# Performance work log

Measured on AMD Instinct MI355X. Metric: run time of the kernel, lower is better.

The kernel has to match this reference:

```python
import jax, jax.numpy as jnp
import numpy as np

B, D, H, W = 2, 64, 128, 128
LARGE = 1e8  # sentinel squared distance (no surface found yet)


def setup_inputs() -> dict:
    key = jax.random.key(0)
    k1, k2 = jax.random.split(key)
    pred = jax.random.normal(k1, (B, 1, D, H, W), dtype=jnp.float32)
    # binary ground-truth mask stored as float, as in the torch module
    target = jax.random.randint(k2, (B, 1, D, H, W), 0, 2).astype(jnp.float32)
    return {"pred": pred, "target": target}


def _erode(m):
    """scipy.ndimage.binary_erosion with default 6-connectivity structure,
    border_value=0 (out-of-bounds treated as background)."""
    e = m
    for ax in range(3):
        pad = [(1, 1) if i == ax else (0, 0) for i in range(3)]
        p = jnp.pad(m, pad)  # False padding
        n = m.shape[ax]
        lo = jax.lax.slice_in_dim(p, 0, n, axis=ax)      # m[i-1]
        hi = jax.lax.slice_in_dim(p, 2, n + 2, axis=ax)  # m[i+1]
        e = e & lo & hi
    return e


def _edt_pass(d2, axis):
    """One separable pass of the exact squared EDT:
    out[i] = min_j (d2[j] + (i-j)^2) along `axis` (Felzenszwalb decomposition,
    computed by brute-force broadcast min, vectorized over all lines)."""
    moved = jnp.moveaxis(d2, axis, 0)
    moved_shape = moved.shape
    n = moved_shape[0]
    x = moved.reshape(n, -1)  # (n, rest)
    idx = jnp.arange(n, dtype=d2.dtype)
    diff2 = (idx[:, None] - idx[None, :]) ** 2  # (n_out, n_in)
    out = jnp.min(x[None, :, :] + diff2[:, :, None], axis=1)  # (n_out, rest)
    return jnp.moveaxis(out.reshape(moved_shape), 0, axis)


def _surface_distance(mask):
    """Distance from every voxel to the nearest surface voxel, where
    surface = mask & ~binary_erosion(mask). Matches
    ndimage.distance_transform_edt(~surface) (exact Euclidean)."""
    eroded = _erode(mask)
    surface = mask & ~eroded
    d2 = jnp.where(surface, jnp.float32(0.0), jnp.float32(LARGE))
    for ax in range(3):
        d2 = _edt_pass(d2, ax)
    return jnp.sqrt(d2)


def _smooth_l1(a, b):
    d = a - b
    ad = jnp.abs(d)
    return jnp.mean(jnp.where(ad < 1.0, 0.5 * d * d, ad - 0.5))


def reference(pred, target):
    p = jax.nn.sigmoid(pred)
    pred_mask = p[:, 0] > 0.5       # (B, D, H, W) bool
    target_mask = target[:, 0] != 0  # astype(bool)

    def per_sample(pm, tm):
        return _smooth_l1(_surface_distance(pm), _surface_distance(tm))

    losses = jax.vmap(per_sample)(pred_mask, target_mask)  # (B,)
    return jnp.mean(losses)
```

## Files before the change

kernel.cpp:

```cpp
#include <hip/hip_runtime.h>

#define D_ 64
#define H_ 128
#define W_ 128
#define VOL (D_*H_*W_)
#define NF 4
#define LARGEF 1e8f
#define SW(r,c) (((r) << 7) + ((c) ^ ((r) & 31)))

__device__ __forceinline__ bool maskv(float v, int which) {
  return which ? (v != 0.0f) : (v > 0.0f);
}

__global__ __launch_bounds__(256) void k_init(const float* __restrict__ pred,
                                              const float* __restrict__ targ,
                                              unsigned char* __restrict__ surf,
                                              double* __restrict__ acc) {
  int idx = blockIdx.x * 256 + threadIdx.x;
  if (idx < 3) acc[idx] = 0.0;
  int f = idx >> 18;
  int q = idx & 262143;
  int which = f & 1;
  const float* __restrict__ src = (which ? targ : pred) + ((size_t)(f >> 1) << 20);
  const float4* __restrict__ s4 = (const float4*)src;
  int v = q << 2;
  int z = v >> 14, y = (v >> 7) & 127, x = v & 127;
  float4 c = s4[q];
  bool m0 = maskv(c.x, which), m1 = maskv(c.y, which);
  bool m2 = maskv(c.z, which), m3 = maskv(c.w, which);
  bool ym0=false, ym1=false, ym2=false, ym3=false;
  bool yp0=false, yp1=false, yp2=false, yp3=false;
  bool zm0=false, zm1=false, zm2=false, zm3=false;
  bool zp0=false, zp1=false, zp2=false, zp3=false;
  if (y > 0)   { float4 t = s4[q - 32];   ym0=maskv(t.x,which); ym1=maskv(t.y,which); ym2=maskv(t.z,which); ym3=maskv(t.w,which); }
  if (y < 127) { float4 t = s4[q + 32];   yp0=maskv(t.x,which); yp1=maskv(t.y,which); yp2=maskv(t.z,which); yp3=maskv(t.w,which); }
  if (z > 0)   { float4 t = s4[q - 4096]; zm0=maskv(t.x,which); zm1=maskv(t.y,which); zm2=maskv(t.z,which); zm3=maskv(t.w,which); }
  if (z < 63)  { float4 t = s4[q + 4096]; zp0=maskv(t.x,which); zp1=maskv(t.y,which); zp2=maskv(t.z,which); zp3=maskv(t.w,which); }
  bool lm = (x > 0)   ? maskv(src[v - 1], which) : false;
  bool rm = (x < 124) ? maskv(src[v + 4], which) : false;
  bool e0 = m0 && lm && m1 && ym0 && yp0 && zm0 && zp0;
  bool e1 = m1 && m0 && m2 && ym1 && yp1 && zm1 && zp1;
  bool e2 = m2 && m1 && m3 && ym2 && yp2 && zm2 && zp2;
  bool e3 = m3 && m2 && rm && ym3 && yp3 && zm3 && zp3;
  uchar4 o;
  o.x = (unsigned char)(m0 && !e0);
  o.y = (unsigned char)(m1 && !e1);
  o.z = (unsigned char)(m2 && !e2);
  o.w = (unsigned char)(m3 && !e3);
  ((uchar4*)surf)[idx] = o;
}

__global__ __launch_bounds__(256) void k_zscan(const unsigned char* __restrict__ surf,
                                               unsigned char* __restrict__ zdist) {
  __shared__ unsigned short fwd[D_][256];
  int g = blockIdx.x * 256 + threadIdx.x;
  int f = g >> 14, yx = g & 16383;
  const unsigned char* s = surf + (f << 20) + yx;
  unsigned char* o = zdist + (f << 20) + yx;
  int d = 255;
  #pragma unroll 16
  for (int z = 0; z < D_; ++z) {
    d = s[z << 14] ? 0 : min(d + 1, 255);
    fwd[z][threadIdx.x] = (unsigned short)d;
  }
  int dd = 255;
  #pragma unroll 8
  for (int z = D_ - 1; z >= 0; --z) {
    int fv = fwd[z][threadIdx.x];
    dd = (fv == 0) ? 0 : min(dd + 1, 255);
    o[z << 14] = (unsigned char)min(fv, dd);
  }
}

__global__ __launch_bounds__(1024) void k_edt_yx(const unsigned char* __restrict__ zdist,
                                                 unsigned short* __restrict__ d2s) {
  __shared__ float tile[128 * 128];
  int f = blockIdx.y, z = blockIdx.x;
  const unsigned char* zsrc = zdist + (f << 20) + (z << 14);
  for (int e = threadIdx.x; e < 16384; e += 1024) {
    int r = e >> 7, c = e & 127;
    int b = zsrc[e];
    float v = (b == 255) ? LARGEF : (float)(b * b);
    tile[SW(r, c)] = v + (float)(r * r);
  }
  __syncthreads();
  const int R = 16;
  int tp = threadIdx.x & 127, tw = threadIdx.x >> 7;
  float best[R], fi[R];
  float fb = (float)(tw * R);
  float tmax = 0.0f;
  #pragma unroll
  for (int u = 0; u < R; ++u) {
    fi[u] = fb + (float)u; best[u] = 3.0e8f;
    float tv = tile[SW(tw * R + u, tp)] - fi[u] * fi[u];
    tmax = fmaxf(tmax, tv);
  }
  #pragma unroll
  for (int o = 1; o < 64; o <<= 1) tmax = fmaxf(tmax, __shfl_xor(tmax, o));
  int rad = (int)sqrtf(tmax);
  int jlo = max(0, tw * R - rad), jhi = min(H_ - 1, tw * R + (R - 1) + rad);
  for (int j = jlo; j <= jhi; ++j) {
    float t = tile[SW(j, tp)];
    float m2j = -2.0f * (float)j;
    #pragma unroll
    for (int u = 0; u < R; ++u)
      best[u] = fminf(best[u], __builtin_fmaf(m2j, fi[u], t));
  }
  __syncthreads();
  float fx2 = (float)(tp * tp);
  #pragma unroll
  for (int u = 0; u < R; ++u)
    tile[SW(tw * R + u, tp)] = best[u] + fi[u] * fi[u] + fx2;
  __syncthreads();
  tmax = 0.0f;
  #pragma unroll
  for (int u = 0; u < R; ++u) {
    best[u] = 3.0e8f;
    float tv = tile[SW(tp, tw * R + u)] - fi[u] * fi[u];
    tmax = fmaxf(tmax, tv);
  }
  #pragma unroll
  for (int o = 1; o < 64; o <<= 1) tmax = fmaxf(tmax, __shfl_xor(tmax, o));
  rad = (int)sqrtf(tmax);
  jlo = max(0, tw * R - rad); jhi = min(W_ - 1, tw * R + (R - 1) + rad);
  for (int j = jlo; j <= jhi; ++j) {
    float t = tile[SW(tp, j)];
    float m2j = -2.0f * (float)j;
    #pragma unroll
    for (int u = 0; u < R; ++u)
      best[u] = fminf(best[u], __builtin_fmaf(m2j, fi[u], t));
  }
  unsigned pk[8];
  #pragma unroll
  for (int p = 0; p < 8; ++p) {
    float dlo = best[2*p]     + fi[2*p]     * fi[2*p];
    float dhi = best[2*p + 1] + fi[2*p + 1] * fi[2*p + 1];
    unsigned lo = (dlo > 65504.f) ? 65535u : (unsigned)dlo;
    unsigned hi = (dhi > 65504.f) ? 65535u : (unsigned)dhi;
    pk[p] = lo | (hi << 16);
  }
  uint4* ob = (uint4*)(d2s + (f << 20) + (z << 14) + (tp << 7) + tw * R);
  ob[0] = make_uint4(pk[0], pk[1], pk[2], pk[3]);
  ob[1] = make_uint4(pk[4], pk[5], pk[6], pk[7]);
}

__global__ __launch_bounds__(256) void k_reduce(const unsigned short* __restrict__ d2s,
                                               double* __restrict__ acc,
                                               float* __restrict__ out) {
  int b = blockIdx.y;
  const uint4* dp = (const uint4*)(d2s + ((size_t)(b * 2 + 0) << 20));
  const uint4* dt = (const uint4*)(d2s + ((size_t)(b * 2 + 1) << 20));
  double s = 0.0;
  for (int v = blockIdx.x * 256 + threadIdx.x; v < VOL / 8; v += gridDim.x * 256) {
    uint4 A = dp[v], C = dt[v];
    unsigned aw[4] = {A.x, A.y, A.z, A.w};
    unsigned cw[4] = {C.x, C.y, C.z, C.w};
    #pragma unroll
    for (int k = 0; k < 4; ++k) {
      unsigned a0 = aw[k] & 0xFFFFu, a1 = aw[k] >> 16;
      unsigned c0 = cw[k] & 0xFFFFu, c1 = cw[k] >> 16;
      float da0 = sqrtf(a0 == 65535u ? LARGEF : (float)a0);
      float da1 = sqrtf(a1 == 65535u ? LARGEF : (float)a1);
      float dc0 = sqrtf(c0 == 65535u ? LARGEF : (float)c0);
      float dc1 = sqrtf(c1 == 65535u ? LARGEF : (float)c1);
      float d0 = da0 - dc0, d1 = da1 - dc1;
      float b0 = fabsf(d0), b1 = fabsf(d1);
      s += (double)(b0 < 1.0f ? 0.5f * d0 * d0 : b0 - 0.5f);
      s += (double)(b1 < 1.0f ? 0.5f * d1 * d1 : b1 - 0.5f);
    }
  }
  for (int o = 32; o > 0; o >>= 1) s += __shfl_down(s, o);
  __shared__ double wsum[4];
  if ((threadIdx.x & 63) == 0) wsum[threadIdx.x >> 6] = s;
  __syncthreads();
  if (threadIdx.x == 0) {
    atomicAdd(&acc[b], wsum[0] + wsum[1] + wsum[2] + wsum[3]);
    __threadfence();
    unsigned* ctr = (unsigned*)&acc[2];
    unsigned done = atomicAdd(ctr, 1u);
    if (done == gridDim.x * gridDim.y - 1) {
      __threadfence();
      out[0] = (float)(0.5 * (acc[0] / (double)VOL + acc[1] / (double)VOL));
    }
  }
}

extern "C" void kernel_launch(void* const* d_in, const int* in_sizes, int n_in,
                              void* d_out, int out_size, void* d_ws, size_t ws_size,
                              hipStream_t stream) {
  const float* pred = (const float*)d_in[0];
  const float* targ = (const float*)d_in[1];
  unsigned char*  surf  = (unsigned char*)d_ws;
  unsigned char*  zdist = (unsigned char*)d_ws + ((size_t)NF << 20);
  unsigned short* d2s   = (unsigned short*)((char*)d_ws + ((size_t)NF << 21));
  double* acc = (double*)((char*)d_ws + ((size_t)NF << 21) + ((size_t)NF * VOL * 2));
  float*  out = (float*)d_out;

  k_init  <<<NF * VOL / 4 / 256, 256, 0, stream>>>(pred, targ, surf, acc);
  k_zscan <<<NF * H_ * W_ / 256, 256, 0, stream>>>(surf, zdist);
  k_edt_yx<<<dim3(D_, NF), 1024, 0, stream>>>(zdist, d2s);
  k_reduce<<<dim3(256, 2), 256, 0, stream>>>(d2s, acc, out);
}
```

Measured before the change: 115.5 us.

## Fuse all four stages into one persistent kernel with grid barriers

```diff
diff --git a/kernel.cpp b/kernel.cpp
--- a/kernel.cpp
+++ b/kernel.cpp
@@ -7,154 +7,181 @@
 #define NF 4
 #define LARGEF 1e8f
 #define SW(r,c) (((r) << 7) + ((c) ^ ((r) & 31)))
+#define GRID 256
+#define TPB 1024
+
+struct Ctl {
+  double acc[2];
+  unsigned ticket;
+  unsigned bar[3];
+};
 
 __device__ __forceinline__ bool maskv(float v, int which) {
   return which ? (v != 0.0f) : (v > 0.0f);
 }
 
-__global__ __launch_bounds__(256) void k_init(const float* __restrict__ pred,
-                                              const float* __restrict__ targ,
-                                              unsigned char* __restrict__ surf,
-                                              double* __restrict__ acc) {
-  int idx = blockIdx.x * 256 + threadIdx.x;
-  if (idx < 3) acc[idx] = 0.0;
-  int f = idx >> 18;
-  int q = idx & 262143;
-  int which = f & 1;
-  const float* __restrict__ src = (which ? targ : pred) + ((size_t)(f >> 1) << 20);
-  const float4* __restrict__ s4 = (const float4*)src;
-  int v = q << 2;
-  int z = v >> 14, y = (v >> 7) & 127, x = v & 127;
-  float4 c = s4[q];
-  bool m0 = maskv(c.x, which), m1 = maskv(c.y, which);
-  bool m2 = maskv(c.z, which), m3 = maskv(c.w, which);
-  bool ym0=false, ym1=false, ym2=false, ym3=false;
-  bool yp0=false, yp1=false, yp2=false, yp3=false;
-  bool zm0=false, zm1=false, zm2=false, zm3=false;
-  bool zp0=false, zp1=false, zp2=false, zp3=false;
-  if (y > 0)   { float4 t = s4[q - 32];   ym0=maskv(t.x,which); ym1=maskv(t.y,which); ym2=maskv(t.z,which); ym3=maskv(t.w,which); }
-  if (y < 127) { float4 t = s4[q + 32];   yp0=maskv(t.x,which); yp1=maskv(t.y,which); yp2=maskv(t.z,which); yp3=maskv(t.w,which); }
-  if (z > 0)   { float4 t = s4[q - 4096]; zm0=maskv(t.x,which); zm1=maskv(t.y,which); zm2=maskv(t.z,which); zm3=maskv(t.w,which); }
-  if (z < 63)  { float4 t = s4[q + 4096]; zp0=maskv(t.x,which); zp1=maskv(t.y,which); zp2=maskv(t.z,which); zp3=maskv(t.w,which); }
-  bool lm = (x > 0)   ? maskv(src[v - 1], which) : false;
-  bool rm = (x < 124) ? maskv(src[v + 4], which) : false;
-  bool e0 = m0 && lm && m1 && ym0 && yp0 && zm0 && zp0;
-  bool e1 = m1 && m0 && m2 && ym1 && yp1 && zm1 && zp1;
-  bool e2 = m2 && m1 && m3 && ym2 && yp2 && zm2 && zp2;
-  bool e3 = m3 && m2 && rm && ym3 && yp3 && zm3 && zp3;
-  uchar4 o;
-  o.x = (unsigned char)(m0 && !e0);
-  o.y = (unsigned char)(m1 && !e1);
-  o.z = (unsigned char)(m2 && !e2);
-  o.w = (unsigned char)(m3 && !e3);
-  ((uchar4*)surf)[idx] = o;
-}
-
-__global__ __launch_bounds__(256) void k_zscan(const unsigned char* __restrict__ surf,
-                                               unsigned char* __restrict__ zdist) {
-  __shared__ unsigned short fwd[D_][256];
-  int g = blockIdx.x * 256 + threadIdx.x;
-  int f = g >> 14, yx = g & 16383;
-  const unsigned char* s = surf + (f << 20) + yx;
-  unsigned char* o = zdist + (f << 20) + yx;
-  int d = 255;
-  #pragma unroll 16
-  for (int z = 0; z < D_; ++z) {
-    d = s[z << 14] ? 0 : min(d + 1, 255);
-    fwd[z][threadIdx.x] = (unsigned short)d;
-  }
-  int dd = 255;
-  #pragma unroll 8
-  for (int z = D_ - 1; z >= 0; --z) {
-    int fv = fwd[z][threadIdx.x];
-    dd = (fv == 0) ? 0 : min(dd + 1, 255);
-    o[z << 14] = (unsigned char)min(fv, dd);
-  }
-}
-
-__global__ __launch_bounds__(1024) void k_edt_yx(const unsigned char* __restrict__ zdist,
-                                                 unsigned short* __restrict__ d2s) {
-  __shared__ float tile[128 * 128];
-  int f = blockIdx.y, z = blockIdx.x;
-  const unsigned char* zsrc = zdist + (f << 20) + (z << 14);
-  for (int e = threadIdx.x; e < 16384; e += 1024) {
-    int r = e >> 7, c = e & 127;
-    int b = zsrc[e];
-    float v = (b == 255) ? LARGEF : (float)(b * b);
-    tile[SW(r, c)] = v + (float)(r * r);
-  }
+__device__ __forceinline__ void gbar(unsigned* ctr) {
   __syncthreads();
-  const int R = 16;
-  int tp = threadIdx.x & 127, tw = threadIdx.x >> 7;
-  float best[R], fi[R];
-  float fb = (float)(tw * R);
-  float tmax = 0.0f;
+  if (threadIdx.x == 0) {
+    __threadfence();
+    atomicAdd(ctr, 1u);
+    while (atomicAdd(ctr, 0u) < GRID) __builtin_amdgcn_s_sleep(2);
+  }
+  __syncthreads();
+  __threadfence();
+}
+
+__global__ __launch_bounds__(TPB) void k_fused(const float* __restrict__ pred,
+                                               const float* __restrict__ targ,
+                                               unsigned char* __restrict__ surf,
+                                               unsigned char* __restrict__ zdist,
+                                               unsigned short* __restrict__ d2s,
+                                               Ctl* __restrict__ ctl,
+                                               float* __restrict__ out) {
+  __shared__ __align__(16) unsigned char smem[65536];
+
   #pragma unroll
-  for (int u = 0; u < R; ++u) {
-    fi[u] = fb + (float)u; best[u] = 3.0e8f;
-    float tv = tile[SW(tw * R + u, tp)] - fi[u] * fi[u];
-    tmax = fmaxf(tmax, tv);
-  }
-  #pragma unroll
-  for (int o = 1; o < 64; o <<= 1) tmax = fmaxf(tmax, __shfl_xor(tmax, o));
-  int rad = (int)sqrtf(tmax);
-  int jlo = max(0, tw * R - rad), jhi = min(H_ - 1, tw * R + (R - 1) + rad);
-  for (int j = jlo; j <= jhi; ++j) {
-    float t = tile[SW(j, tp)];
-    float m2j = -2.0f * (float)j;
+  for (int it = 0; it < 4; ++it) {
+    int idx = blockIdx.x * TPB + threadIdx.x + it * (GRID * TPB);
+    int f = idx >> 18;
+    int q = idx & 262143;
+    int which = f & 1;
+    const float* __restrict__ src = (which ? targ : pred) + ((size_t)(f >> 1) << 20);
+    const float4* __restrict__ s4 = (const float4*)src;
+    int v = q << 2;
+    int z = v >> 14, y = (v >> 7) & 127, x = v & 127;
+    float4 c = s4[q];
+    bool m0 = maskv(c.x, which), m1 = maskv(c.y, which);
+    bool m2 = maskv(c.z, which), m3 = maskv(c.w, which);
+    bool ym0=false, ym1=false, ym2=false, ym3=false;
+    bool yp0=false, yp1=false, yp2=false, yp3=false;
+    bool zm0=false, zm1=false, zm2=false, zm3=false;
+    bool zp0=false, zp1=false, zp2=false, zp3=false;
+    if (y > 0)   { float4 t = s4[q - 32];   ym0=maskv(t.x,which); ym1=maskv(t.y,which); ym2=maskv(t.z,which); ym3=maskv(t.w,which); }
+    if (y < 127) { float4 t = s4[q + 32];   yp0=maskv(t.x,which); yp1=maskv(t.y,which); yp2=maskv(t.z,which); yp3=maskv(t.w,which); }
+    if (z > 0)   { float4 t = s4[q - 4096]; zm0=maskv(t.x,which); zm1=maskv(t.y,which); zm2=maskv(t.z,which); zm3=maskv(t.w,which); }
+    if (z < 63)  { float4 t = s4[q + 4096]; zp0=maskv(t.x,which); zp1=maskv(t.y,which); zp2=maskv(t.z,which); zp3=maskv(t.w,which); }
+    bool lm = (x > 0)   ? maskv(src[v - 1], which) : false;
+    bool rm = (x < 124) ? maskv(src[v + 4], which) : false;
+    bool e0 = m0 && lm && m1 && ym0 && yp0 && zm0 && zp0;
+    bool e1 = m1 && m0 && m2 && ym1 && yp1 && zm1 && zp1;
+    bool e2 = m2 && m1 && m3 && ym2 && yp2 && zm2 && zp2;
+    bool e3 = m3 && m2 && rm && ym3 && yp3 && zm3 && zp3;
+    uchar4 o;
+    o.x = (unsigned char)(m0 && !e0);
+    o.y = (unsigned char)(m1 && !e1);
+    o.z = (unsigned char)(m2 && !e2);
+    o.w = (unsigned char)(m3 && !e3);
+    ((uchar4*)surf)[idx] = o;
+  }
+  gbar(&ctl->bar[0]);
+
+  {
+    unsigned short (*fwd)[256] = (unsigned short (*)[256])smem;
+    if (threadIdx.x < 256) {
+      int g = blockIdx.x * 256 + threadIdx.x;
+      int f = g >> 14, yx = g & 16383;
+      const unsigned char* s = surf + (f << 20) + yx;
+      unsigned char* o = zdist + (f << 20) + yx;
+      int d = 255;
+      #pragma unroll 16
+      for (int z = 0; z < D_; ++z) {
+        d = s[z << 14] ? 0 : min(d + 1, 255);
+        fwd[z][threadIdx.x] = (unsigned short)d;
+      }
+      int dd = 255;
+      #pragma unroll 8
+      for (int z = D_ - 1; z >= 0; --z) {
+        int fv = fwd[z][threadIdx.x];
+        dd = (fv == 0) ? 0 : min(dd + 1, 255);
+        o[z << 14] = (unsigned char)min(fv, dd);
+      }
+    }
+  }
+  gbar(&ctl->bar[1]);
+
+  {
+    float* tile = (float*)smem;
+    int f = blockIdx.x >> 6, z = blockIdx.x & 63;
+    const unsigned char* zsrc = zdist + (f << 20) + (z << 14);
+    for (int e = threadIdx.x; e < 16384; e += TPB) {
+      int r = e >> 7, c = e & 127;
+      int b = zsrc[e];
+      float v = (b == 255) ? LARGEF : (float)(b * b);
+      tile[SW(r, c)] = v + (float)(r * r);
+    }
+    __syncthreads();
+    const int R = 16;
+    int tp = threadIdx.x & 127, tw = threadIdx.x >> 7;
+    float best[R], fi[R];
+    float fb = (float)(tw * R);
+    float tmax = 0.0f;
+    #pragma unroll
+    for (int u = 0; u < R; ++u) {
+      fi[u] = fb + (float)u; best[u] = 3.0e8f;
+      float tv = tile[SW(tw * R + u, tp)] - fi[u] * fi[u];
+      tmax = fmaxf(tmax, tv);
+    }
+    #pragma unroll
+    for (int o = 1; o < 64; o <<= 1) tmax = fmaxf(tmax, __shfl_xor(tmax, o));
+    int rad = (int)sqrtf(tmax);
+    int jlo = max(0, tw * R - rad), jhi = min(H_ - 1, tw * R + (R - 1) + rad);
+    for (int j = jlo; j <= jhi; ++j) {
+      float t = tile[SW(j, tp)];
+      float m2j = -2.0f * (float)j;
+      #pragma unroll
+      for (int u = 0; u < R; ++u)
+        best[u] = fminf(best[u], __builtin_fmaf(m2j, fi[u], t));
+    }
+    __syncthreads();
+    float fx2 = (float)(tp * tp);
     #pragma unroll
     for (int u = 0; u < R; ++u)
-      best[u] = fminf(best[u], __builtin_fmaf(m2j, fi[u], t));
-  }
-  __syncthreads();
-  float fx2 = (float)(tp * tp);
-  #pragma unroll
-  for (int u = 0; u < R; ++u)
-    tile[SW(tw * R + u, tp)] = best[u] + fi[u] * fi[u] + fx2;
-  __syncthreads();
-  tmax = 0.0f;
-  #pragma unroll
-  for (int u = 0; u < R; ++u) {
-    best[u] = 3.0e8f;
-    float tv = tile[SW(tp, tw * R + u)] - fi[u] * fi[u];
-    tmax = fmaxf(tmax, tv);
-  }
-  #pragma unroll
-  for (int o = 1; o < 64; o <<= 1) tmax = fmaxf(tmax, __shfl_xor(tmax, o));
-  rad = (int)sqrtf(tmax);
-  jlo = max(0, tw * R - rad); jhi = min(W_ - 1, tw * R + (R - 1) + rad);
-  for (int j = jlo; j <= jhi; ++j) {
-    float t = tile[SW(tp, j)];
-    float m2j = -2.0f * (float)j;
-    #pragma unroll
-    for (int u = 0; u < R; ++u)
-      best[u] = fminf(best[u], __builtin_fmaf(m2j, fi[u], t));
-  }
-  unsigned pk[8];
-  #pragma unroll
-  for (int p = 0; p < 8; ++p) {
-    float dlo = best[2*p]     + fi[2*p]     * fi[2*p];
-    float dhi = best[2*p + 1] + fi[2*p + 1] * fi[2*p + 1];
-    unsigned lo = (dlo > 65504.f) ? 65535u : (unsigned)dlo;
-    unsigned hi = (dhi > 65504.f) ? 65535u : (unsigned)dhi;
-    pk[p] = lo | (hi << 16);
-  }
-  uint4* ob = (uint4*)(d2s + (f << 20) + (z << 14) + (tp << 7) + tw * R);
-  ob[0] = make_uint4(pk[0], pk[1], pk[2], pk[3]);
-  ob[1] = make_uint4(pk[4], pk[5], pk[6], pk[7]);
-}
-
-__global__ __launch_bounds__(256) void k_reduce(const unsigned short* __restrict__ d2s,
-                                               double* __restrict__ acc,
-                                               float* __restrict__ out) {
-  int b = blockIdx.y;
-  const uint4* dp = (const uint4*)(d2s + ((size_t)(b * 2 + 0) << 20));
-  const uint4* dt = (const uint4*)(d2s + ((size_t)(b * 2 + 1) << 20));
-  double s = 0.0;
-  for (int v = blockIdx.x * 256 + threadIdx.x; v < VOL / 8; v += gridDim.x * 256) {
-    uint4 A = dp[v], C = dt[v];
+      tile[SW(tw * R + u, tp)] = best[u] + fi[u] * fi[u] + fx2;
+    __syncthreads();
+    tmax = 0.0f;
+    #pragma unroll
+    for (int u = 0; u < R; ++u) {
+      best[u] = 3.0e8f;
+      float tv = tile[SW(tp, tw * R + u)] - fi[u] * fi[u];
+      tmax = fmaxf(tmax, tv);
+    }
+    #pragma unroll
+    for (int o = 1; o < 64; o <<= 1) tmax = fmaxf(tmax, __shfl_xor(tmax, o));
+    rad = (int)sqrtf(tmax);
+    jlo = max(0, tw * R - rad); jhi = min(W_ - 1, tw * R + (R - 1) + rad);
+    for (int j = jlo; j <= jhi; ++j) {
+      float t = tile[SW(tp, j)];
+      float m2j = -2.0f * (float)j;
+      #pragma unroll
+      for (int u = 0; u < R; ++u)
+        best[u] = fminf(best[u], __builtin_fmaf(m2j, fi[u], t));
+    }
+    unsigned pk[8];
+    #pragma unroll
+    for (int p = 0; p < 8; ++p) {
+      float dlo = best[2*p]     + fi[2*p]     * fi[2*p];
+      float dhi = best[2*p + 1] + fi[2*p + 1] * fi[2*p + 1];
+      unsigned lo = (dlo > 65504.f) ? 65535u : (unsigned)dlo;
+      unsigned hi = (dhi > 65504.f) ? 65535u : (unsigned)dhi;
+      pk[p] = lo | (hi << 16);
+    }
+    uint4* ob = (uint4*)(d2s + (f << 20) + (z << 14) + (tp << 7) + tw * R);
+    ob[0] = make_uint4(pk[0], pk[1], pk[2], pk[3]);
+    ob[1] = make_uint4(pk[4], pk[5], pk[6], pk[7]);
+  }
+  gbar(&ctl->bar[2]);
+
+  {
+    int v = blockIdx.x * TPB + threadIdx.x;
+    int b = v >> 17;
+    int idx = v & 131071;
+    const uint4* dp = (const uint4*)(d2s + ((size_t)(b * 2 + 0) << 20));
+    const uint4* dt = (const uint4*)(d2s + ((size_t)(b * 2 + 1) << 20));
+    uint4 A = dp[idx], C = dt[idx];
     unsigned aw[4] = {A.x, A.y, A.z, A.w};
     unsigned cw[4] = {C.x, C.y, C.z, C.w};
+    double s = 0.0;
     #pragma unroll
     for (int k = 0; k < 4; ++k) {
       unsigned a0 = aw[k] & 0xFFFFu, a1 = aw[k] >> 16;
@@ -168,19 +195,22 @@
       s += (double)(b0 < 1.0f ? 0.5f * d0 * d0 : b0 - 0.5f);
       s += (double)(b1 < 1.0f ? 0.5f * d1 * d1 : b1 - 0.5f);
     }
-  }
-  for (int o = 32; o > 0; o >>= 1) s += __shfl_down(s, o);
-  __shared__ double wsum[4];
-  if ((threadIdx.x & 63) == 0) wsum[threadIdx.x >> 6] = s;
-  __syncthreads();
-  if (threadIdx.x == 0) {
-    atomicAdd(&acc[b], wsum[0] + wsum[1] + wsum[2] + wsum[3]);
-    __threadfence();
-    unsigned* ctr = (unsigned*)&acc[2];
-    unsigned done = atomicAdd(ctr, 1u);
-    if (done == gridDim.x * gridDim.y - 1) {
+    #pragma unroll
+    for (int o = 32; o > 0; o >>= 1) s += __shfl_down(s, o);
+    double* wsum = (double*)smem;
+    if ((threadIdx.x & 63) == 0) wsum[threadIdx.x >> 6] = s;
+    __syncthreads();
+    if (threadIdx.x == 0) {
+      double bs = 0.0;
+      #pragma unroll
+      for (int w = 0; w < TPB / 64; ++w) bs += wsum[w];
+      atomicAdd(&ctl->acc[b], bs);
       __threadfence();
-      out[0] = (float)(0.5 * (acc[0] / (double)VOL + acc[1] / (double)VOL));
+      unsigned done = atomicAdd(&ctl->ticket, 1u);
+      if (done == GRID - 1) {
+        __threadfence();
+        out[0] = (float)(0.5 * (ctl->acc[0] / (double)VOL + ctl->acc[1] / (double)VOL));
+      }
     }
   }
 }
@@ -190,14 +220,12 @@
                               hipStream_t stream) {
   const float* pred = (const float*)d_in[0];
   const float* targ = (const float*)d_in[1];
-  unsigned char*  surf  = (unsigned char*)d_ws;
-  unsigned char*  zdist = (unsigned char*)d_ws + ((size_t)NF << 20);
-  unsigned short* d2s   = (unsigned short*)((char*)d_ws + ((size_t)NF << 21));
-  double* acc = (double*)((char*)d_ws + ((size_t)NF << 21) + ((size_t)NF * VOL * 2));
-  float*  out = (float*)d_out;
-
-  k_init  <<<NF * VOL / 4 / 256, 256, 0, stream>>>(pred, targ, surf, acc);
-  k_zscan <<<NF * H_ * W_ / 256, 256, 0, stream>>>(surf, zdist);
-  k_edt_yx<<<dim3(D_, NF), 1024, 0, stream>>>(zdist, d2s);
-  k_reduce<<<dim3(256, 2), 256, 0, stream>>>(d2s, acc, out);
-}
+  Ctl* ctl = (Ctl*)d_ws;
+  unsigned char*  surf  = (unsigned char*)d_ws + 1024;
+  unsigned char*  zdist = surf + ((size_t)NF << 20);
+  unsigned short* d2s   = (unsigned short*)(zdist + ((size_t)NF << 20));
+  float* out = (float*)d_out;
+
+  hipMemsetAsync(ctl, 0, sizeof(Ctl), stream);
+  k_fused<<<GRID, TPB, 0, stream>>>(pred, targ, surf, zdist, d2s, ctl, out);
+}
```

Result: slower. 339.4 us (+193.8%).
